# Performance work log

Measured on AMD Instinct MI355X. Metric: run time of the kernel, lower is better.

The kernel has to match this reference:

```python
import jax, jax.numpy as jnp
import numpy as np

N = 100000
E = 1600000
D_IN = 64
D_H = 64
D_OUT = 10
G = 512
EPS = 1e-5


def setup_inputs() -> dict:
    key = jax.random.key(0)
    ks = jax.random.split(key, 12)
    x = jax.random.normal(ks[0], (N, D_IN), dtype=jnp.float32)
    edge_index = jax.random.randint(ks[1], (2, E), 0, N, dtype=jnp.int64)
    batch = jnp.sort(jax.random.randint(ks[2], (N,), 0, G, dtype=jnp.int64))

    def glorot(k, fan_in, fan_out):
        lim = float(np.sqrt(6.0 / (fan_in + fan_out)))
        return jax.random.uniform(k, (fan_in, fan_out), jnp.float32, -lim, lim)

    params = {
        'W1': glorot(ks[3], D_IN, D_H), 'b1': jnp.zeros((D_H,), jnp.float32),
        'g1': jnp.ones((D_H,), jnp.float32), 'be1': jnp.zeros((D_H,), jnp.float32),
        'W2': glorot(ks[4], D_H, D_H), 'b2': jnp.zeros((D_H,), jnp.float32),
        'g2': jnp.ones((D_H,), jnp.float32), 'be2': jnp.zeros((D_H,), jnp.float32),
        'W3': glorot(ks[5], D_H, D_H), 'b3': jnp.zeros((D_H,), jnp.float32),
        'g3': jnp.ones((D_H,), jnp.float32), 'be3': jnp.zeros((D_H,), jnp.float32),
        'Wfc': glorot(ks[6], D_H, D_OUT), 'bfc': jnp.zeros((D_OUT,), jnp.float32),
    }
    return dict(x=x, edge_index=edge_index, batch=batch, **params)


def _gcn_prep(edge_index):
    # add self-loops, compute symmetric degree normalization (PyG GCNConv)
    loop = jnp.arange(N, dtype=edge_index.dtype)
    src = jnp.concatenate([edge_index[0], loop])  # [E+N]
    dst = jnp.concatenate([edge_index[1], loop])
    deg = jax.ops.segment_sum(jnp.ones_like(dst, dtype=jnp.float32), dst, num_segments=N)
    dinv = jnp.where(deg > 0, jax.lax.rsqrt(deg), 0.0)
    norm = dinv[src] * dinv[dst]  # [E+N]
    return src, dst, norm


def _gcn_conv(x, src, dst, norm, W, b):
    h = x @ W                                   # [N, D]
    msg = h[src] * norm[:, None]                # gather + scale [E+N, D]
    out = jax.ops.segment_sum(msg, dst, num_segments=N)  # scatter-add
    return out + b


def _bn_relu(x, gamma, beta):
    # BatchNorm1d with batch statistics (training mode, biased variance)
    mu = jnp.mean(x, axis=0)
    var = jnp.mean(jnp.square(x - mu), axis=0)
    y = (x - mu) * jax.lax.rsqrt(var + EPS) * gamma + beta
    return jax.nn.relu(y)


def reference(x, edge_index, batch, W1, b1, g1, be1, W2, b2, g2, be2,
              W3, b3, g3, be3, Wfc, bfc):
    src, dst, norm = _gcn_prep(edge_index)
    # dropout treated as identity (eval-mode) for deterministic reference
    h = _bn_relu(_gcn_conv(x, src, dst, norm, W1, b1), g1, be1)
    h = _bn_relu(_gcn_conv(h, src, dst, norm, W2, b2), g2, be2)
    h = _bn_relu(_gcn_conv(h, src, dst, norm, W3, b3), g3, be3)
    # global mean pool over graphs
    sums = jax.ops.segment_sum(h, batch, num_segments=G)       # [G, D]
    cnt = jax.ops.segment_sum(jnp.ones((N,), jnp.float32), batch, num_segments=G)
    pooled = sums / jnp.maximum(cnt, 1.0)[:, None]
    return pooled @ Wfc + bfc  # [G, D_OUT]
```

## Files before the change

kernel.cpp:

```cpp
#include <hip/hip_runtime.h>

#define NNODES 100000
#define NEDGES 1600000
#define DH 64
#define NG 512
#define DOUT 10
#define EPSV 1e-5f
#define SCAN_BLKS 391
#define PCH 128
#define NB 196
#define EBLK 4096
#define NEB 391

typedef short bf16x8 __attribute__((ext_vector_type(8)));
typedef float f32x4 __attribute__((ext_vector_type(4)));

__device__ inline unsigned bf16_rne(float x) {
    unsigned u = __float_as_uint(x);
    return (u + 0x7fffu + ((u >> 16) & 1u)) >> 16;
}
__device__ inline float bflo(unsigned u) { return __uint_as_float(u << 16); }
__device__ inline float bfhi(unsigned u) { return __uint_as_float(u & 0xffff0000u); }

__global__ void k_zero(int* __restrict__ cntdeg, float* __restrict__ pooled,
                       int* __restrict__ gstart, int* __restrict__ gend,
                       float* __restrict__ stats) {
    int i = blockIdx.x * 256 + threadIdx.x;
    if (i < NNODES) cntdeg[i] = 0;
    if (i < NG * DH) pooled[i] = 0.0f;
    if (i < NG) { gstart[i] = 0; gend[i] = 0; }
    if (i < 384) stats[i] = 0.0f;
}

__global__ void k_count(const int* __restrict__ dstE, int* __restrict__ cntdeg) {
    int e2 = blockIdx.x * 256 + threadIdx.x;
    if (e2 * 2 + 1 < NEDGES) {
        int2 d = ((const int2*)dstE)[e2];
        atomicAdd(&cntdeg[d.x], 1);
        atomicAdd(&cntdeg[d.y], 1);
    } else if (e2 * 2 < NEDGES) {
        atomicAdd(&cntdeg[dstE[e2 * 2]], 1);
    }
}

__global__ void k_scan1(const int* __restrict__ cntdeg, int* __restrict__ bsum,
                        float* __restrict__ dinv, const int* __restrict__ batch,
                        int* __restrict__ gstart, int* __restrict__ gend) {
    __shared__ int ls[256];
    int t = threadIdx.x, i = blockIdx.x * 256 + t;
    int v = (i < NNODES) ? cntdeg[i] : 0;
    if (i < NNODES) {
        dinv[i] = rsqrtf(1.0f + (float)v);
        int g = batch[i];
        if (i == 0 || batch[i - 1] != g) gstart[g] = i;
        if (i == NNODES - 1 || batch[i + 1] != g) gend[g] = i + 1;
    }
    ls[t] = v;
    __syncthreads();
#pragma unroll
    for (int off = 128; off > 0; off >>= 1) {
        if (t < off) ls[t] += ls[t + off];
        __syncthreads();
    }
    if (t == 0) bsum[blockIdx.x] = ls[0];
}

__global__ void __launch_bounds__(512) k_scan2(const int* __restrict__ bsum,
                                               int* __restrict__ boff) {
    __shared__ int ps[512];
    int t = threadIdx.x;
    int v = (t < SCAN_BLKS) ? bsum[t] : 0;
    ps[t] = v;
    __syncthreads();
#pragma unroll
    for (int off = 1; off < 512; off <<= 1) {
        int u = (t >= off) ? ps[t - off] : 0;
        __syncthreads();
        ps[t] += u;
        __syncthreads();
    }
    if (t < SCAN_BLKS) boff[t] = ps[t] - v;
}

__global__ void k_scan3(const int* __restrict__ cntdeg, const int* __restrict__ boff,
                        int* __restrict__ rowptr) {
    __shared__ int ps[256];
    int t = threadIdx.x, i = blockIdx.x * 256 + t;
    int v = (i < NNODES) ? cntdeg[i] : 0;
    ps[t] = v;
    __syncthreads();
#pragma unroll
    for (int off = 1; off < 256; off <<= 1) {
        int u = (t >= off) ? ps[t - off] : 0;
        __syncthreads();
        ps[t] += u;
        __syncthreads();
    }
    if (i < NNODES) rowptr[i] = boff[blockIdx.x] + ps[t] - v;
    if (i == 0) rowptr[NNODES] = NEDGES;
}

__global__ void k_hist(const int* __restrict__ dstE, int* __restrict__ bhist) {
    __shared__ int lc[NB];
    int t = threadIdx.x, eb = blockIdx.x;
    for (int j = t; j < NB; j += 256) lc[j] = 0;
    __syncthreads();
    int e0 = eb * EBLK;
#pragma unroll
    for (int k = 0; k < EBLK / 256; ++k) {
        int e = e0 + k * 256 + t;
        if (e < NEDGES) atomicAdd(&lc[dstE[e] >> 9], 1);
    }
    __syncthreads();
    for (int j = t; j < NB; j += 256) bhist[eb * NB + j] = lc[j];
}

__global__ void __launch_bounds__(512) k_bscan(const int* __restrict__ bhist,
                                               const int* __restrict__ rowptr,
                                               int* __restrict__ boffs) {
    __shared__ int ps[512];
    int b = blockIdx.x, t = threadIdx.x;
    int v = (t < NEB) ? bhist[t * NB + b] : 0;
    ps[t] = v;
    __syncthreads();
#pragma unroll
    for (int off = 1; off < 512; off <<= 1) {
        int u = (t >= off) ? ps[t - off] : 0;
        __syncthreads();
        ps[t] += u;
        __syncthreads();
    }
    if (t < NEB) boffs[t * NB + b] = rowptr[b << 9] + ps[t] - v;
}

__global__ void k_bucket(const int* __restrict__ srcE, const int* __restrict__ dstE,
                         const int* __restrict__ boffs, int2* __restrict__ staged) {
    __shared__ int lc[NB];
    __shared__ int lb[NB];
    int t = threadIdx.x, eb = blockIdx.x;
    for (int j = t; j < NB; j += 256) { lc[j] = 0; lb[j] = boffs[eb * NB + j]; }
    __syncthreads();
    int e0 = eb * EBLK;
#pragma unroll
    for (int k = 0; k < EBLK / 256; ++k) {
        int e = e0 + k * 256 + t;
        if (e < NEDGES) {
            int d = dstE[e], s = srcE[e];
            int b = d >> 9;
            int slot = atomicAdd(&lc[b], 1);
            staged[lb[b] + slot] = make_int2(s, d);
        }
    }
}

__global__ void k_fill2(const int2* __restrict__ staged, const int* __restrict__ rowptr,
                        int* __restrict__ csr4) {
    __shared__ int cur[512];
    int b = blockIdx.x, t = threadIdx.x;
    int n0 = b << 9;
    int nCnt = NNODES - n0;
    if (nCnt > 512) nCnt = 512;
    for (int j = t; j < nCnt; j += 256) cur[j] = rowptr[n0 + j];
    __syncthreads();
    int base = rowptr[n0], end = rowptr[n0 + nCnt];
    for (int e = base + t; e < end; e += 256) {
        int2 sd = staged[e];
        int pos = atomicAdd(&cur[sd.y - n0], 1);
        csr4[pos] = sd.x;
    }
}

__global__ void k_wprep(const float* __restrict__ W0, const float* __restrict__ W1,
                        const float* __restrict__ W2, short* __restrict__ wf) {
    int t = blockIdx.x * 256 + threadIdx.x;
    if (t >= 1536) return;
    int layer = t >> 9;
    int rem = t & 511;
    int ct = rem >> 7, ks = (rem >> 6) & 1, lane = rem & 63;
    const float* W = (layer == 0) ? W0 : (layer == 1) ? W1 : W2;
    short* hi = wf + layer * 8192 + rem * 8;
    short* lo = hi + 4096;
#pragma unroll
    for (int i = 0; i < 8; ++i) {
        int k = ks * 32 + ((lane >> 4) << 3) + i;
        int n = ct * 16 + (lane & 15);
        float v = W[k * 64 + n];
        unsigned h = bf16_rne(v);
        float fh = __uint_as_float(h << 16);
        unsigned l = bf16_rne(v - fh);
        hi[i] = (short)h;
        lo[i] = (short)l;
    }
}

template <int AFFINE>
__global__ void __launch_bounds__(256) k_mgemm(const float* __restrict__ in,
        const short* __restrict__ wf, const float* __restrict__ scale,
        const float* __restrict__ shift, unsigned short* __restrict__ out) {
    const int tid = threadIdx.x;
    const int wv = tid >> 6, l = tid & 63;
    const int r0 = blockIdx.x * 64 + wv * 16;
    const int row = r0 + (l & 15);
    const int kq = (l >> 4) << 3;

    float a[2][8];
    if (row < NNODES) {
        const float* rp = in + (size_t)row * 64 + kq;
        *(float4*)&a[0][0] = *(const float4*)(rp);
        *(float4*)&a[0][4] = *(const float4*)(rp + 4);
        *(float4*)&a[1][0] = *(const float4*)(rp + 32);
        *(float4*)&a[1][4] = *(const float4*)(rp + 36);
    } else {
#pragma unroll
        for (int ks = 0; ks < 2; ++ks)
#pragma unroll
            for (int i = 0; i < 8; ++i) a[ks][i] = 0.0f;
    }
    if (AFFINE) {
#pragma unroll
        for (int ks = 0; ks < 2; ++ks) {
            float4 sc0 = *(const float4*)(scale + kq + ks * 32);
            float4 sc1 = *(const float4*)(scale + kq + ks * 32 + 4);
            float4 sh0 = *(const float4*)(shift + kq + ks * 32);
            float4 sh1 = *(const float4*)(shift + kq + ks * 32 + 4);
            a[ks][0] = fmaxf(fmaf(a[ks][0], sc0.x, sh0.x), 0.0f);
            a[ks][1] = fmaxf(fmaf(a[ks][1], sc0.y, sh0.y), 0.0f);
            a[ks][2] = fmaxf(fmaf(a[ks][2], sc0.z, sh0.z), 0.0f);
            a[ks][3] = fmaxf(fmaf(a[ks][3], sc0.w, sh0.w), 0.0f);
            a[ks][4] = fmaxf(fmaf(a[ks][4], sc1.x, sh1.x), 0.0f);
            a[ks][5] = fmaxf(fmaf(a[ks][5], sc1.y, sh1.y), 0.0f);
            a[ks][6] = fmaxf(fmaf(a[ks][6], sc1.z, sh1.z), 0.0f);
            a[ks][7] = fmaxf(fmaf(a[ks][7], sc1.w, sh1.w), 0.0f);
        }
    }

    bf16x8 ah[2], al[2];
#pragma unroll
    for (int ks = 0; ks < 2; ++ks)
#pragma unroll
        for (int i = 0; i < 8; ++i) {
            unsigned h = bf16_rne(a[ks][i]);
            float fh = __uint_as_float(h << 16);
            ah[ks][i] = (short)h;
            al[ks][i] = (short)bf16_rne(a[ks][i] - fh);
        }

    const int rb = r0 + ((l >> 4) << 2);
    const int cb = l & 15;
#pragma unroll
    for (int ct = 0; ct < 4; ++ct) {
        const short* base = wf + (ct * 128 + l) * 8;
        bf16x8 wh0 = *(const bf16x8*)(base);
        bf16x8 wh1 = *(const bf16x8*)(base + 64 * 8);
        bf16x8 wl0 = *(const bf16x8*)(base + 4096);
        bf16x8 wl1 = *(const bf16x8*)(base + 4096 + 64 * 8);
        f32x4 acc = {0.0f, 0.0f, 0.0f, 0.0f};
        acc = __builtin_amdgcn_mfma_f32_16x16x32_bf16(ah[0], wh0, acc, 0, 0, 0);
        acc = __builtin_amdgcn_mfma_f32_16x16x32_bf16(ah[1], wh1, acc, 0, 0, 0);
        acc = __builtin_amdgcn_mfma_f32_16x16x32_bf16(al[0], wh0, acc, 0, 0, 0);
        acc = __builtin_amdgcn_mfma_f32_16x16x32_bf16(al[1], wh1, acc, 0, 0, 0);
        acc = __builtin_amdgcn_mfma_f32_16x16x32_bf16(ah[0], wl0, acc, 0, 0, 0);
        acc = __builtin_amdgcn_mfma_f32_16x16x32_bf16(ah[1], wl1, acc, 0, 0, 0);
        int n = ct * 16 + cb;
#pragma unroll
        for (int r = 0; r < 4; ++r)
            if (rb + r < NNODES) out[(size_t)(rb + r) * 64 + n] = (unsigned short)bf16_rne(acc[r]);
    }
}

__global__ void k_gather(const uint4* __restrict__ h, const int* __restrict__ csr4,
                         const int* __restrict__ rowptr, const float* __restrict__ dinv,
                         const float* __restrict__ bias, float* __restrict__ agg) {
    int t = blockIdx.x * 256 + threadIdx.x;
    int i = t >> 3, q = t & 7;
    if (i >= NNODES) return;
    float dv = dinv[i];
    uint4 hv = h[(size_t)i * 8 + q];
    float A[8], B[8];
    A[0] = bflo(hv.x) * dv; A[1] = bfhi(hv.x) * dv;
    A[2] = bflo(hv.y) * dv; A[3] = bfhi(hv.y) * dv;
    A[4] = bflo(hv.z) * dv; A[5] = bfhi(hv.z) * dv;
    A[6] = bflo(hv.w) * dv; A[7] = bfhi(hv.w) * dv;
#pragma unroll
    for (int k = 0; k < 8; ++k) B[k] = 0.0f;

    int e0 = rowptr[i], e1 = rowptr[i + 1];
    int e = e0;
    for (; e + 4 <= e1; e += 4) {
        int sa = csr4[e], sb = csr4[e + 1], sc = csr4[e + 2], sd = csr4[e + 3];
        float na = dinv[sa], nb = dinv[sb], nc = dinv[sc], nd = dinv[sd];
        uint4 va = h[(size_t)sa * 8 + q];
        uint4 vb = h[(size_t)sb * 8 + q];
        uint4 vc = h[(size_t)sc * 8 + q];
        uint4 vd = h[(size_t)sd * 8 + q];
        A[0] = fmaf(bflo(va.x), na, A[0]); A[1] = fmaf(bfhi(va.x), na, A[1]);
        A[2] = fmaf(bflo(va.y), na, A[2]); A[3] = fmaf(bfhi(va.y), na, A[3]);
        A[4] = fmaf(bflo(va.z), na, A[4]); A[5] = fmaf(bfhi(va.z), na, A[5]);
        A[6] = fmaf(bflo(va.w), na, A[6]); A[7] = fmaf(bfhi(va.w), na, A[7]);
        B[0] = fmaf(bflo(vb.x), nb, B[0]); B[1] = fmaf(bfhi(vb.x), nb, B[1]);
        B[2] = fmaf(bflo(vb.y), nb, B[2]); B[3] = fmaf(bfhi(vb.y), nb, B[3]);
        B[4] = fmaf(bflo(vb.z), nb, B[4]); B[5] = fmaf(bfhi(vb.z), nb, B[5]);
        B[6] = fmaf(bflo(vb.w), nb, B[6]); B[7] = fmaf(bfhi(vb.w), nb, B[7]);
        A[0] = fmaf(bflo(vc.x), nc, A[0]); A[1] = fmaf(bfhi(vc.x), nc, A[1]);
        A[2] = fmaf(bflo(vc.y), nc, A[2]); A[3] = fmaf(bfhi(vc.y), nc, A[3]);
        A[4] = fmaf(bflo(vc.z), nc, A[4]); A[5] = fmaf(bfhi(vc.z), nc, A[5]);
        A[6] = fmaf(bflo(vc.w), nc, A[6]); A[7] = fmaf(bfhi(vc.w), nc, A[7]);
        B[0] = fmaf(bflo(vd.x), nd, B[0]); B[1] = fmaf(bfhi(vd.x), nd, B[1]);
        B[2] = fmaf(bflo(vd.y), nd, B[2]); B[3] = fmaf(bfhi(vd.y), nd, B[3]);
        B[4] = fmaf(bflo(vd.z), nd, B[4]); B[5] = fmaf(bfhi(vd.z), nd, B[5]);
        B[6] = fmaf(bflo(vd.w), nd, B[6]); B[7] = fmaf(bfhi(vd.w), nd, B[7]);
    }
    for (; e + 2 <= e1; e += 2) {
        int sa = csr4[e], sb = csr4[e + 1];
        float na = dinv[sa], nb = dinv[sb];
        uint4 va = h[(size_t)sa * 8 + q];
        uint4 vb = h[(size_t)sb * 8 + q];
        A[0] = fmaf(bflo(va.x), na, A[0]); A[1] = fmaf(bfhi(va.x), na, A[1]);
        A[2] = fmaf(bflo(va.y), na, A[2]); A[3] = fmaf(bfhi(va.y), na, A[3]);
        A[4] = fmaf(bflo(va.z), na, A[4]); A[5] = fmaf(bfhi(va.z), na, A[5]);
        A[6] = fmaf(bflo(va.w), na, A[6]); A[7] = fmaf(bfhi(va.w), na, A[7]);
        B[0] = fmaf(bflo(vb.x), nb, B[0]); B[1] = fmaf(bfhi(vb.x), nb, B[1]);
        B[2] = fmaf(bflo(vb.y), nb, B[2]); B[3] = fmaf(bfhi(vb.y), nb, B[3]);
        B[4] = fmaf(bflo(vb.z), nb, B[4]); B[5] = fmaf(bfhi(vb.z), nb, B[5]);
        B[6] = fmaf(bflo(vb.w), nb, B[6]); B[7] = fmaf(bfhi(vb.w), nb, B[7]);
    }
    if (e < e1) {
        int sa = csr4[e];
        float na = dinv[sa];
        uint4 va = h[(size_t)sa * 8 + q];
        A[0] = fmaf(bflo(va.x), na, A[0]); A[1] = fmaf(bfhi(va.x), na, A[1]);
        A[2] = fmaf(bflo(va.y), na, A[2]); A[3] = fmaf(bfhi(va.y), na, A[3]);
        A[4] = fmaf(bflo(va.z), na, A[4]); A[5] = fmaf(bfhi(va.z), na, A[5]);
        A[6] = fmaf(bflo(va.w), na, A[6]); A[7] = fmaf(bfhi(va.w), na, A[7]);
    }
    float4 b0 = ((const float4*)bias)[q * 2];
    float4 b1 = ((const float4*)bias)[q * 2 + 1];
    float4 r0, r1;
    r0.x = fmaf(A[0] + B[0], dv, b0.x); r0.y = fmaf(A[1] + B[1], dv, b0.y);
    r0.z = fmaf(A[2] + B[2], dv, b0.z); r0.w = fmaf(A[3] + B[3], dv, b0.w);
    r1.x = fmaf(A[4] + B[4], dv, b1.x); r1.y = fmaf(A[5] + B[5], dv, b1.y);
    r1.z = fmaf(A[6] + B[6], dv, b1.z); r1.w = fmaf(A[7] + B[7], dv, b1.w);
    ((float4*)agg)[(size_t)i * 16 + q * 2] = r0;
    ((float4*)agg)[(size_t)i * 16 + q * 2 + 1] = r1;
}

__global__ void k_stats(const float* __restrict__ agg, float* __restrict__ stats) {
    const int tid = threadIdx.x;
    const int c4 = (tid & 15) * 4;
    const int rg = tid >> 4;
    float s0 = 0, s1 = 0, s2 = 0, s3 = 0;
    float q0 = 0, q1 = 0, q2 = 0, q3 = 0;
    for (int r = blockIdx.x * 16 + rg; r < NNODES; r += gridDim.x * 16) {
        float4 v = *(const float4*)(agg + (size_t)r * 64 + c4);
        s0 += v.x; s1 += v.y; s2 += v.z; s3 += v.w;
        q0 = fmaf(v.x, v.x, q0); q1 = fmaf(v.y, v.y, q1);
        q2 = fmaf(v.z, v.z, q2); q3 = fmaf(v.w, v.w, q3);
    }
    __shared__ float ls[16 * 64], lq[16 * 64];
    ls[rg * 64 + c4 + 0] = s0; ls[rg * 64 + c4 + 1] = s1;
    ls[rg * 64 + c4 + 2] = s2; ls[rg * 64 + c4 + 3] = s3;
    lq[rg * 64 + c4 + 0] = q0; lq[rg * 64 + c4 + 1] = q1;
    lq[rg * 64 + c4 + 2] = q2; lq[rg * 64 + c4 + 3] = q3;
    __syncthreads();
    if (tid < 64) {
        float s = 0, q = 0;
#pragma unroll
        for (int g = 0; g < 16; ++g) {
            s += ls[g * 64 + tid];
            q += lq[g * 64 + tid];
        }
        unsafeAtomicAdd(&stats[tid], s);
        unsafeAtomicAdd(&stats[64 + tid], q);
    }
}

__global__ void k_bnparams(const float* __restrict__ stats, const float* __restrict__ g,
                           const float* __restrict__ be, float* __restrict__ scale,
                           float* __restrict__ shift) {
    int c = threadIdx.x;
    if (c < 64) {
        float mu = stats[c] * (1.0f / NNODES);
        float var = stats[64 + c] * (1.0f / NNODES) - mu * mu;
        float sc = g[c] * rsqrtf(var + EPSV);
        scale[c] = sc;
        shift[c] = fmaf(-mu, sc, be[c]);
    }
}

__global__ void k_pool(const float* __restrict__ agg, const float* __restrict__ scale,
                       const float* __restrict__ shift, const int* __restrict__ batch,
                       float* __restrict__ pooled) {
    const int tid = threadIdx.x;
    const int c = tid & 63, r = tid >> 6;
    const int i0 = blockIdx.x * PCH;
    const float sc = scale[c], sh = shift[c];
    float acc = 0.0f;
    int cur = -1;
#pragma unroll 4
    for (int k = 0; k < PCH / 4; ++k) {
        int i = i0 + k * 4 + r;
        if (i >= NNODES) break;
        int g = batch[i];
        if (g != cur) {
            if (cur >= 0) unsafeAtomicAdd(&pooled[cur * 64 + c], acc);
            acc = 0.0f;
            cur = g;
        }
        acc += fmaxf(fmaf(agg[(size_t)i * 64 + c], sc, sh), 0.0f);
    }
    if (cur >= 0) unsafeAtomicAdd(&pooled[cur * 64 + c], acc);
}

__global__ void k_final(const float* __restrict__ pooled, const int* __restrict__ gstart,
                        const int* __restrict__ gend, const float* __restrict__ Wfc,
                        const float* __restrict__ bfc, float* __restrict__ out) {
    __shared__ float p[64];
    __shared__ float ic;
    int g = blockIdx.x, tid = threadIdx.x;
    p[tid] = pooled[(size_t)g * 64 + tid];
    if (tid == 0) ic = 1.0f / fmaxf((float)(gend[g] - gstart[g]), 1.0f);
    __syncthreads();
    if (tid < DOUT) {
        float a = bfc[tid];
#pragma unroll 8
        for (int c = 0; c < 64; ++c) a = fmaf(p[c] * ic, Wfc[c * DOUT + tid], a);
        out[g * DOUT + tid] = a;
    }
}

extern "C" void kernel_launch(void* const* d_in, const int* in_sizes, int n_in,
                              void* d_out, int out_size, void* d_ws, size_t ws_size,
                              hipStream_t stream) {
    const float* x = (const float*)d_in[0];
    const int* ei = (const int*)d_in[1];
    const int* batch = (const int*)d_in[2];
    const int* srcE = ei;
    const int* dstE = ei + NEDGES;
    const float* W[3] = {(const float*)d_in[3], (const float*)d_in[7], (const float*)d_in[11]};
    const float* B[3] = {(const float*)d_in[4], (const float*)d_in[8], (const float*)d_in[12]};
    const float* Gm[3] = {(const float*)d_in[5], (const float*)d_in[9], (const float*)d_in[13]};
    const float* Be[3] = {(const float*)d_in[6], (const float*)d_in[10], (const float*)d_in[14]};
    const float* Wfc = (const float*)d_in[15];
    const float* bfc = (const float*)d_in[16];
    float* out = (float*)d_out;

    float* f = (float*)d_ws;
    float* dinv = f;
    int* cntdeg = (int*)(f + 100000);
    int* rowptr = (int*)(f + 200000);
    int* csr4 = (int*)(f + 400016);
    unsigned short* h = (unsigned short*)(f + 2000016);
    float* agg = f + 5200016;
    float* stats = agg + (size_t)NNODES * DH;
    float* scale = stats + 384;
    float* shift = scale + 64;
    float* pooled = shift + 64;
    int* gstart = (int*)(pooled + NG * DH);
    int* gend = gstart + NG;
    short* wf = (short*)(gend + NG);
    int* bsum = (int*)((short*)wf + 24576);
    int* boff = bsum + 400;
    int* bhist = boff + 400;
    int* boffs = bhist + NEB * NB;
    int2* staged = (int2*)(f + 11800882);

    k_zero<<<(NNODES + 255) / 256, 256, 0, stream>>>(cntdeg, pooled, gstart, gend, stats);
    k_count<<<(NEDGES / 2 + 255) / 256, 256, 0, stream>>>(dstE, cntdeg);
    k_scan1<<<SCAN_BLKS, 256, 0, stream>>>(cntdeg, bsum, dinv, batch, gstart, gend);
    k_scan2<<<1, 512, 0, stream>>>(bsum, boff);
    k_scan3<<<SCAN_BLKS, 256, 0, stream>>>(cntdeg, boff, rowptr);
    k_hist<<<NEB, 256, 0, stream>>>(dstE, bhist);
    k_bscan<<<NB, 512, 0, stream>>>(bhist, rowptr, boffs);
    k_bucket<<<NEB, 256, 0, stream>>>(srcE, dstE, boffs, staged);
    k_fill2<<<NB, 256, 0, stream>>>(staged, rowptr, csr4);
    k_wprep<<<6, 256, 0, stream>>>(W[0], W[1], W[2], wf);

    const int gemm_grid = (NNODES + 63) / 64;
    for (int l = 0; l < 3; ++l) {
        const float* in = (l == 0) ? x : agg;
        if (l == 0)
            k_mgemm<0><<<gemm_grid, 256, 0, stream>>>(in, wf + l * 8192, scale, shift, h);
        else
            k_mgemm<1><<<gemm_grid, 256, 0, stream>>>(in, wf + l * 8192, scale, shift, h);
        k_gather<<<(NNODES * 8 + 255) / 256, 256, 0, stream>>>((const uint4*)h, csr4, rowptr, dinv, B[l], agg);
        k_stats<<<512, 256, 0, stream>>>(agg, stats + l * 128);
        k_bnparams<<<1, 64, 0, stream>>>(stats + l * 128, Gm[l], Be[l], scale, shift);
    }

    k_pool<<<(NNODES + PCH - 1) / PCH, 256, 0, stream>>>(agg, scale, shift, batch, pooled);
    k_final<<<NG, 64, 0, stream>>>(pooled, gstart, gend, Wfc, bfc, out);
}
```

Before: 490.7 us.

## Derive CSR rowptr and degrees from bucket histograms, drop global atomic count and scans

Removes the global atomic degree count and the three-pass prefix scan over nodes. Bucket totals now come from the existing per-block histograms through a single-block scan. Each fill block counts per-node degrees in shared memory, scans them locally, and writes rowptr and dinv itself. This trades the global atomics and several launches for an extra pass over staged edges per bucket and a serial single-block reduction over 391 histogram rows.

```diff
diff --git a/kernel.cpp b/kernel.cpp
--- a/kernel.cpp
+++ b/kernel.cpp
@@ -6,7 +6,6 @@
 #define NG 512
 #define DOUT 10
 #define EPSV 1e-5f
-#define SCAN_BLKS 391
 #define PCH 128
 #define NB 196
 #define EBLK 4096
@@ -22,82 +21,21 @@
 __device__ inline float bflo(unsigned u) { return __uint_as_float(u << 16); }
 __device__ inline float bfhi(unsigned u) { return __uint_as_float(u & 0xffff0000u); }
 
-__global__ void k_zero(int* __restrict__ cntdeg, float* __restrict__ pooled,
-                       int* __restrict__ gstart, int* __restrict__ gend,
-                       float* __restrict__ stats) {
+__global__ void k_zero(float* __restrict__ pooled, int* __restrict__ gstart,
+                       int* __restrict__ gend, float* __restrict__ stats) {
     int i = blockIdx.x * 256 + threadIdx.x;
-    if (i < NNODES) cntdeg[i] = 0;
     if (i < NG * DH) pooled[i] = 0.0f;
     if (i < NG) { gstart[i] = 0; gend[i] = 0; }
     if (i < 384) stats[i] = 0.0f;
 }
 
-__global__ void k_count(const int* __restrict__ dstE, int* __restrict__ cntdeg) {
-    int e2 = blockIdx.x * 256 + threadIdx.x;
-    if (e2 * 2 + 1 < NEDGES) {
-        int2 d = ((const int2*)dstE)[e2];
-        atomicAdd(&cntdeg[d.x], 1);
-        atomicAdd(&cntdeg[d.y], 1);
-    } else if (e2 * 2 < NEDGES) {
-        atomicAdd(&cntdeg[dstE[e2 * 2]], 1);
-    }
-}
-
-__global__ void k_scan1(const int* __restrict__ cntdeg, int* __restrict__ bsum,
-                        float* __restrict__ dinv, const int* __restrict__ batch,
-                        int* __restrict__ gstart, int* __restrict__ gend) {
-    __shared__ int ls[256];
-    int t = threadIdx.x, i = blockIdx.x * 256 + t;
-    int v = (i < NNODES) ? cntdeg[i] : 0;
-    if (i < NNODES) {
-        dinv[i] = rsqrtf(1.0f + (float)v);
-        int g = batch[i];
-        if (i == 0 || batch[i - 1] != g) gstart[g] = i;
-        if (i == NNODES - 1 || batch[i + 1] != g) gend[g] = i + 1;
-    }
-    ls[t] = v;
-    __syncthreads();
-#pragma unroll
-    for (int off = 128; off > 0; off >>= 1) {
-        if (t < off) ls[t] += ls[t + off];
-        __syncthreads();
-    }
-    if (t == 0) bsum[blockIdx.x] = ls[0];
-}
-
-__global__ void __launch_bounds__(512) k_scan2(const int* __restrict__ bsum,
-                                               int* __restrict__ boff) {
-    __shared__ int ps[512];
-    int t = threadIdx.x;
-    int v = (t < SCAN_BLKS) ? bsum[t] : 0;
-    ps[t] = v;
-    __syncthreads();
-#pragma unroll
-    for (int off = 1; off < 512; off <<= 1) {
-        int u = (t >= off) ? ps[t - off] : 0;
-        __syncthreads();
-        ps[t] += u;
-        __syncthreads();
-    }
-    if (t < SCAN_BLKS) boff[t] = ps[t] - v;
-}
-
-__global__ void k_scan3(const int* __restrict__ cntdeg, const int* __restrict__ boff,
-                        int* __restrict__ rowptr) {
-    __shared__ int ps[256];
-    int t = threadIdx.x, i = blockIdx.x * 256 + t;
-    int v = (i < NNODES) ? cntdeg[i] : 0;
-    ps[t] = v;
-    __syncthreads();
-#pragma unroll
-    for (int off = 1; off < 256; off <<= 1) {
-        int u = (t >= off) ? ps[t - off] : 0;
-        __syncthreads();
-        ps[t] += u;
-        __syncthreads();
-    }
-    if (i < NNODES) rowptr[i] = boff[blockIdx.x] + ps[t] - v;
-    if (i == 0) rowptr[NNODES] = NEDGES;
+__global__ void k_batch(const int* __restrict__ batch, int* __restrict__ gstart,
+                        int* __restrict__ gend) {
+    int i = blockIdx.x * 256 + threadIdx.x;
+    if (i >= NNODES) return;
+    int g = batch[i];
+    if (i == 0 || batch[i - 1] != g) gstart[g] = i;
+    if (i == NNODES - 1 || batch[i + 1] != g) gend[g] = i + 1;
 }
 
 __global__ void k_hist(const int* __restrict__ dstE, int* __restrict__ bhist) {
@@ -115,8 +53,28 @@
     for (int j = t; j < NB; j += 256) bhist[eb * NB + j] = lc[j];
 }
 
+__global__ void __launch_bounds__(256) k_btot(const int* __restrict__ bhist,
+                                              int* __restrict__ bucketbase) {
+    __shared__ int ps[256];
+    int t = threadIdx.x;
+    int s = 0;
+    if (t < NB)
+        for (int eb = 0; eb < NEB; ++eb) s += bhist[eb * NB + t];
+    ps[t] = s;
+    __syncthreads();
+#pragma unroll
+    for (int off = 1; off < 256; off <<= 1) {
+        int u = (t >= off) ? ps[t - off] : 0;
+        __syncthreads();
+        ps[t] += u;
+        __syncthreads();
+    }
+    if (t < NB) bucketbase[t] = ps[t] - s;
+    if (t == 0) bucketbase[NB] = NEDGES;
+}
+
 __global__ void __launch_bounds__(512) k_bscan(const int* __restrict__ bhist,
-                                               const int* __restrict__ rowptr,
+                                               const int* __restrict__ bucketbase,
                                                int* __restrict__ boffs) {
     __shared__ int ps[512];
     int b = blockIdx.x, t = threadIdx.x;
@@ -130,7 +88,7 @@
         ps[t] += u;
         __syncthreads();
     }
-    if (t < NEB) boffs[t * NB + b] = rowptr[b << 9] + ps[t] - v;
+    if (t < NEB) boffs[t * NB + b] = bucketbase[b] + ps[t] - v;
 }
 
 __global__ void k_bucket(const int* __restrict__ srcE, const int* __restrict__ dstE,
@@ -153,21 +111,46 @@
     }
 }
 
-__global__ void k_fill2(const int2* __restrict__ staged, const int* __restrict__ rowptr,
-                        int* __restrict__ csr4) {
+__global__ void __launch_bounds__(512) k_fill3(const int2* __restrict__ staged,
+                                               const int* __restrict__ bucketbase,
+                                               int* __restrict__ rowptr,
+                                               float* __restrict__ dinv,
+                                               int* __restrict__ csr4) {
+    __shared__ int cnt[512];
+    __shared__ int ps[512];
     __shared__ int cur[512];
     int b = blockIdx.x, t = threadIdx.x;
     int n0 = b << 9;
-    int nCnt = NNODES - n0;
-    if (nCnt > 512) nCnt = 512;
-    for (int j = t; j < nCnt; j += 256) cur[j] = rowptr[n0 + j];
-    __syncthreads();
-    int base = rowptr[n0], end = rowptr[n0 + nCnt];
-    for (int e = base + t; e < end; e += 256) {
+    cnt[t] = 0;
+    __syncthreads();
+    int base = bucketbase[b], end = bucketbase[b + 1];
+    for (int e = base + t; e < end; e += 512)
+        atomicAdd(&cnt[staged[e].y - n0], 1);
+    __syncthreads();
+    int v = cnt[t];
+    ps[t] = v;
+    __syncthreads();
+#pragma unroll
+    for (int off = 1; off < 512; off <<= 1) {
+        int u = (t >= off) ? ps[t - off] : 0;
+        __syncthreads();
+        ps[t] += u;
+        __syncthreads();
+    }
+    int ex = base + ps[t] - v;
+    int node = n0 + t;
+    if (node < NNODES) {
+        rowptr[node] = ex;
+        dinv[node] = rsqrtf(1.0f + (float)v);
+    }
+    cur[t] = ex;
+    __syncthreads();
+    for (int e = base + t; e < end; e += 512) {
         int2 sd = staged[e];
         int pos = atomicAdd(&cur[sd.y - n0], 1);
         csr4[pos] = sd.x;
     }
+    if (b == 0 && t == 0) rowptr[NNODES] = NEDGES;
 }
 
 __global__ void k_wprep(const float* __restrict__ W0, const float* __restrict__ W1,
@@ -446,7 +429,6 @@
 
     float* f = (float*)d_ws;
     float* dinv = f;
-    int* cntdeg = (int*)(f + 100000);
     int* rowptr = (int*)(f + 200000);
     int* csr4 = (int*)(f + 400016);
     unsigned short* h = (unsigned short*)(f + 2000016);
@@ -458,21 +440,18 @@
     int* gstart = (int*)(pooled + NG * DH);
     int* gend = gstart + NG;
     short* wf = (short*)(gend + NG);
-    int* bsum = (int*)((short*)wf + 24576);
-    int* boff = bsum + 400;
-    int* bhist = boff + 400;
+    int* bucketbase = (int*)((short*)wf + 24576);
+    int* bhist = bucketbase + 256;
     int* boffs = bhist + NEB * NB;
     int2* staged = (int2*)(f + 11800882);
 
-    k_zero<<<(NNODES + 255) / 256, 256, 0, stream>>>(cntdeg, pooled, gstart, gend, stats);
-    k_count<<<(NEDGES / 2 + 255) / 256, 256, 0, stream>>>(dstE, cntdeg);
-    k_scan1<<<SCAN_BLKS, 256, 0, stream>>>(cntdeg, bsum, dinv, batch, gstart, gend);
-    k_scan2<<<1, 512, 0, stream>>>(bsum, boff);
-    k_scan3<<<SCAN_BLKS, 256, 0, stream>>>(cntdeg, boff, rowptr);
+    k_zero<<<(NG * DH + 255) / 256, 256, 0, stream>>>(pooled, gstart, gend, stats);
+    k_batch<<<(NNODES + 255) / 256, 256, 0, stream>>>(batch, gstart, gend);
     k_hist<<<NEB, 256, 0, stream>>>(dstE, bhist);
-    k_bscan<<<NB, 512, 0, stream>>>(bhist, rowptr, boffs);
+    k_btot<<<1, 256, 0, stream>>>(bhist, bucketbase);
+    k_bscan<<<NB, 512, 0, stream>>>(bhist, bucketbase, boffs);
     k_bucket<<<NEB, 256, 0, stream>>>(srcE, dstE, boffs, staged);
-    k_fill2<<<NB, 256, 0, stream>>>(staged, rowptr, csr4);
+    k_fill3<<<NB, 512, 0, stream>>>(staged, bucketbase, rowptr, dinv, csr4);
     k_wprep<<<6, 256, 0, stream>>>(W[0], W[1], W[2], wf);
 
     const int gemm_grid = (NNODES + 63) / 64;
```

After: 440.0 us. -10.3%, faster.
